# Kernel tuning notes

Hardware: AMD Instinct MI355X
Metric: run time of the kernel (lower is better)

Reference implementation:

```python
import jax, jax.numpy as jnp
import numpy as np

B, H, S, D = 2, 8, 2048, 64  # batch, heads, seq_len, depth (= F_hidden)
LEAKY_SLOPE = 0.2            # tf.nn.leaky_relu default alpha
EPS_ADJ = 1e-9


def setup_inputs() -> dict:
    key = jax.random.key(0)
    ks = jax.random.split(key, 8)
    scale = 1.0 / np.sqrt(D)  # glorot-ish for square [D,D] fan
    return {
        "Hin": jax.random.normal(ks[0], (B, H, S, D), jnp.float32),
        "Hk": jax.random.normal(ks[1], (B, H, S, D), jnp.float32),
        "Hv": jax.random.normal(ks[2], (B, H, S, D), jnp.float32),
        "A": jax.random.normal(ks[3], (B, H, D, D), jnp.float32),
        "mask": jnp.zeros((B, 1, 1, S), jnp.float32),
        "W": jax.random.normal(ks[4], (H, D, D), jnp.float32) * scale,
        "b": jnp.zeros((H, D, D), jnp.float32),
        "a_vec": jax.random.normal(ks[5], (H, D, D), jnp.float32) * scale,
        "ba": jnp.zeros((H, D, D), jnp.float32),
        "pw": jax.random.normal(ks[6], (H, D, D), jnp.float32) * scale,
    }


def reference(Hin, Hk, Hv, A, mask, W, b, a_vec, ba, pw):
    # AW = relu(W @ A + b) + eps          [B,H,D,D]
    AW = jax.nn.relu(jnp.einsum("hfd,bhde->bhfe", W, A) + b[None]) + EPS_ADJ
    # learned power transform on metric tensor
    Ap = AW ** pw[None]                   # [B,H,D,D]
    # energy curvature tensor: a @ Ap + ba
    avAp = jnp.einsum("hfd,bhde->bhfe", a_vec, Ap) + ba[None]  # [B,H,D,D]
    # attention scores: (Hin @ avAp) @ Hk^T / sqrt(dk)
    WHiWHj = jnp.einsum("bhsf,bhfe->bhse", Hin, avAp)          # [B,H,S,D]
    Ep = jnp.einsum("bhse,bhte->bhst", WHiWHj, Hk)             # [B,H,S,S]
    Ep = Ep / jnp.sqrt(jnp.float32(D))
    Ep = jax.nn.leaky_relu(Ep, LEAKY_SLOPE)
    E = jax.nn.softmax(Ep + mask * (-1e9), axis=-1)            # [B,H,S,S]
    # value matmul + output activation (relu); att_head=1 so concat == single head
    H_next = jax.nn.relu(jnp.einsum("bhst,bhtd->bhsd", E, Hv))  # [B,H,S,D]
    return H_next
```

## Files before the change

### kernel.cpp

```cpp
#include <hip/hip_runtime.h>
#include <cmath>

#define B_ 2
#define H_ 8
#define S_ 2048
#define D_ 64
#define TS 64
#define NT (S_ / TS)
#define LDST 68

typedef __attribute__((ext_vector_type(8))) _Float16 f16x8;
typedef __attribute__((ext_vector_type(4))) float f32x4;

__global__ __launch_bounds__(256) void prep_avAp(
    const float* __restrict__ A, const float* __restrict__ W,
    const float* __restrict__ bb, const float* __restrict__ av,
    const float* __restrict__ ba, const float* __restrict__ pw,
    float* __restrict__ avAp)
{
    __shared__ float s0[TS * LDST];
    __shared__ float s1[TS * LDST];
    const int tid = threadIdx.x;
    const int ty = tid >> 4, tx = tid & 15;
    const int bh = blockIdx.x;
    const int h = bh & (H_ - 1);

    const float4* W4 = (const float4*)(W + h * D_ * D_);
    const float4* A4 = (const float4*)(A + bh * D_ * D_);
#pragma unroll
    for (int it = 0; it < 4; ++it) {
        int idx = tid + it * 256;
        int r = idx >> 4, c = idx & 15;
        *(float4*)&s0[r * LDST + c * 4] = W4[idx];
        *(float4*)&s1[r * LDST + c * 4] = A4[idx];
    }
    __syncthreads();

    float acc[4][4] = {};
    for (int d = 0; d < D_; ++d) {
        float4 a4 = *(const float4*)&s1[d * LDST + tx * 4];
#pragma unroll
        for (int i = 0; i < 4; ++i) {
            float w = s0[(ty * 4 + i) * LDST + d];
            acc[i][0] += w * a4.x; acc[i][1] += w * a4.y;
            acc[i][2] += w * a4.z; acc[i][3] += w * a4.w;
        }
    }
    __syncthreads();

#pragma unroll
    for (int i = 0; i < 4; ++i) {
        int f = ty * 4 + i;
        float4 b4 = *(const float4*)&bb[(h * D_ + f) * D_ + tx * 4];
        float4 p4 = *(const float4*)&pw[(h * D_ + f) * D_ + tx * 4];
        float vb[4] = {b4.x, b4.y, b4.z, b4.w};
        float vp[4] = {p4.x, p4.y, p4.z, p4.w};
#pragma unroll
        for (int j = 0; j < 4; ++j) {
            float aw = fmaxf(acc[i][j] + vb[j], 0.f) + 1e-9f;
            s0[f * LDST + tx * 4 + j] = exp2f(vp[j] * __log2f(aw));
        }
    }
    const float4* av4 = (const float4*)(av + h * D_ * D_);
#pragma unroll
    for (int it = 0; it < 4; ++it) {
        int idx = tid + it * 256;
        int r = idx >> 4, c = idx & 15;
        *(float4*)&s1[r * LDST + c * 4] = av4[idx];
    }
    __syncthreads();

    float acc2[4][4] = {};
    for (int d = 0; d < D_; ++d) {
        float4 a4 = *(const float4*)&s0[d * LDST + tx * 4];
#pragma unroll
        for (int i = 0; i < 4; ++i) {
            float w = s1[(ty * 4 + i) * LDST + d];
            acc2[i][0] += w * a4.x; acc2[i][1] += w * a4.y;
            acc2[i][2] += w * a4.z; acc2[i][3] += w * a4.w;
        }
    }
#pragma unroll
    for (int i = 0; i < 4; ++i) {
        int f = ty * 4 + i;
        float4 ba4 = *(const float4*)&ba[(h * D_ + f) * D_ + tx * 4];
        float4 o = make_float4(acc2[i][0] + ba4.x, acc2[i][1] + ba4.y,
                               acc2[i][2] + ba4.z, acc2[i][3] + ba4.w);
        *(float4*)&avAp[bh * D_ * D_ + f * D_ + tx * 4] = o;
    }
}

#define KH_S 0
#define KL_S 8192
#define VT_S 16384
#define P_S  24576
#define MROW_S 32768
#define QP_S 40960
#define AVP_S 0
#define HIN_S 17408
#define SMEM_SZ 58368

__global__ __launch_bounds__(256) void flash4(
    const float* __restrict__ Hin, const float* __restrict__ Hk,
    const float* __restrict__ Hv, const float* __restrict__ maskg,
    const float* __restrict__ avAp, float* __restrict__ out)
{
    __shared__ __align__(16) char smem[SMEM_SZ];
    float* AVP = (float*)(smem + AVP_S);
    float* HIN = (float*)(smem + HIN_S);
    float* QP  = (float*)(smem + QP_S);
    float* MROW = (float*)(smem + MROW_S);

    const int tid = threadIdx.x;
    const int wave = tid >> 6, lane = tid & 63;
    const int l15 = lane & 15, lg = lane >> 4;
    const int qt = blockIdx.x, bh = blockIdx.y;
    const int b = bh >> 3;
    const size_t base = (size_t)bh * S_ * D_;
    const int q0 = qt * TS;

    {
        const float4* a4 = (const float4*)(avAp + bh * D_ * D_);
        const float4* h4 = (const float4*)(Hin + base + (size_t)q0 * D_);
#pragma unroll
        for (int i = 0; i < 4; ++i) {
            int f = tid + i * 256;
            int r = f >> 4, c = (f & 15) * 4;
            *(float4*)&AVP[r * LDST + c] = a4[f];
            *(float4*)&HIN[r * LDST + c] = h4[f];
        }
    }
    __syncthreads();
    {
        const int tx = tid & 15, ty = tid >> 4;
        float acc[4][4] = {};
        for (int d = 0; d < D_; ++d) {
            float4 av = *(const float4*)&AVP[d * LDST + tx * 4];
#pragma unroll
            for (int rr = 0; rr < 4; ++rr) {
                float h = HIN[(ty * 4 + rr) * LDST + d];
                acc[rr][0] += h * av.x; acc[rr][1] += h * av.y;
                acc[rr][2] += h * av.z; acc[rr][3] += h * av.w;
            }
        }
#pragma unroll
        for (int rr = 0; rr < 4; ++rr)
            *(float4*)&QP[(ty * 4 + rr) * LDST + tx * 4] =
                make_float4(acc[rr][0], acc[rr][1], acc[rr][2], acc[rr][3]);
    }
    __syncthreads();

    f16x8 qAh[2], qAl[2];
#pragma unroll
    for (int kc = 0; kc < 2; ++kc) {
        int row = wave * 16 + l15;
        int k0 = kc * 32 + lg * 8;
        float4 v0 = *(const float4*)&QP[row * LDST + k0];
        float4 v1 = *(const float4*)&QP[row * LDST + k0 + 4];
        float xs[8] = {v0.x, v0.y, v0.z, v0.w, v1.x, v1.y, v1.z, v1.w};
#pragma unroll
        for (int j = 0; j < 8; ++j) {
            float x = xs[j] * 0.125f;
            _Float16 hh = (_Float16)x;
            qAh[kc][j] = hh;
            qAl[kc][j] = (_Float16)(x - (float)hh);
        }
    }

    float4 kreg[2][2], vreg[2][2];
    auto stage_load = [&](int kt) {
        const float* Kg = Hk + base + (size_t)kt * TS * D_;
        const float* Vg = Hv + base + (size_t)kt * TS * D_;
#pragma unroll
        for (int i = 0; i < 2; ++i) {
            int c = tid + i * 256;
            kreg[i][0] = *(const float4*)(Kg + c * 8);
            kreg[i][1] = *(const float4*)(Kg + c * 8 + 4);
            vreg[i][0] = *(const float4*)(Vg + c * 8);
            vreg[i][1] = *(const float4*)(Vg + c * 8 + 4);
        }
    };
    auto stage_write = [&]() {
#pragma unroll
        for (int i = 0; i < 2; ++i) {
            int c = tid + i * 256;
            int r = c >> 3, c8 = c & 7;
            float xs[8] = {kreg[i][0].x, kreg[i][0].y, kreg[i][0].z, kreg[i][0].w,
                           kreg[i][1].x, kreg[i][1].y, kreg[i][1].z, kreg[i][1].w};
            f16x8 h, l;
#pragma unroll
            for (int e = 0; e < 8; ++e) {
                _Float16 hh = (_Float16)xs[e];
                h[e] = hh; l[e] = (_Float16)(xs[e] - (float)hh);
            }
            int byte = (r * 128 + c8 * 16) ^ ((r & 7) << 4);
            *(f16x8*)(smem + KH_S + byte) = h;
            *(f16x8*)(smem + KL_S + byte) = l;
            float vs[8] = {vreg[i][0].x, vreg[i][0].y, vreg[i][0].z, vreg[i][0].w,
                           vreg[i][1].x, vreg[i][1].y, vreg[i][1].z, vreg[i][1].w};
#pragma unroll
            for (int e = 0; e < 8; ++e) {
                int vr = c8 * 8 + e;
                int vb = (vr * 128 + r * 2) ^
                         ((((vr & 7) ^ ((vr >> 3) & 7)) << 4));
                *(_Float16*)(smem + VT_S + vb) = (_Float16)vs[e];
            }
        }
    };

    stage_load(0);
    stage_write();
    for (int i = tid; i < S_; i += 256) MROW[i] = -1e9f * maskg[b * S_ + i];
    __syncthreads();

    float mrun[4], lrun[4];
    f32x4 o[4];
#pragma unroll
    for (int i = 0; i < 4; ++i) {
        mrun[i] = -INFINITY; lrun[i] = 0.f;
        o[i] = (f32x4){0.f, 0.f, 0.f, 0.f};
    }

    for (int kt = 0; kt < NT; ++kt) {
        if (kt + 1 < NT) stage_load(kt + 1);

        f32x4 s[4];
#pragma unroll
        for (int ns = 0; ns < 4; ++ns) s[ns] = (f32x4){0.f, 0.f, 0.f, 0.f};
        __builtin_amdgcn_s_setprio(1);
#pragma unroll
        for (int ns = 0; ns < 4; ++ns)
#pragma unroll
            for (int kc = 0; kc < 2; ++kc) {
                int row = ns * 16 + l15;
                int byte = (row * 128 + kc * 64 + lg * 16) ^ ((row & 7) << 4);
                f16x8 kh = *(const f16x8*)(smem + KH_S + byte);
                f16x8 kl = *(const f16x8*)(smem + KL_S + byte);
                s[ns] = __builtin_amdgcn_mfma_f32_16x16x32_f16(qAh[kc], kh, s[ns], 0, 0, 0);
                s[ns] = __builtin_amdgcn_mfma_f32_16x16x32_f16(qAl[kc], kh, s[ns], 0, 0, 0);
                s[ns] = __builtin_amdgcn_mfma_f32_16x16x32_f16(qAh[kc], kl, s[ns], 0, 0, 0);
            }
        __builtin_amdgcn_s_setprio(0);

        float mk[4];
#pragma unroll
        for (int ns = 0; ns < 4; ++ns) mk[ns] = MROW[kt * 64 + ns * 16 + l15];
        float scs[4];
#pragma unroll
        for (int r = 0; r < 4; ++r) {
            float v[4];
#pragma unroll
            for (int ns = 0; ns < 4; ++ns) {
                float x = s[ns][r];
                x = (x > 0.f) ? x : 0.2f * x;
                v[ns] = x + mk[ns];
            }
            float m0 = fmaxf(fmaxf(v[0], v[1]), fmaxf(v[2], v[3]));
#pragma unroll
            for (int off = 1; off < 16; off <<= 1)
                m0 = fmaxf(m0, __shfl_xor(m0, off, 64));
            float mnew = fmaxf(mrun[r], m0);
            float sc = __expf(mrun[r] - mnew);
            mrun[r] = mnew;
            float rs = 0.f;
            float p[4];
#pragma unroll
            for (int ns = 0; ns < 4; ++ns) { p[ns] = __expf(v[ns] - mnew); rs += p[ns]; }
#pragma unroll
            for (int off = 1; off < 16; off <<= 1)
                rs += __shfl_xor(rs, off, 64);
            lrun[r] = lrun[r] * sc + rs;
            scs[r] = sc;
            int prow = lg * 4 + r;
#pragma unroll
            for (int ns = 0; ns < 4; ++ns) {
                int pb = (prow * 128 + (ns * 16 + l15) * 2) ^ ((prow & 7) << 4);
                *(_Float16*)(smem + P_S + wave * 2048 + pb) = (_Float16)p[ns];
            }
        }
#pragma unroll
        for (int ns = 0; ns < 4; ++ns)
#pragma unroll
            for (int r = 0; r < 4; ++r) o[ns][r] *= scs[r];

        __syncthreads();

        __builtin_amdgcn_s_setprio(1);
#pragma unroll
        for (int kc = 0; kc < 2; ++kc) {
            int pb = (l15 * 128 + kc * 64 + lg * 16) ^ ((l15 & 7) << 4);
            f16x8 pf = *(const f16x8*)(smem + P_S + wave * 2048 + pb);
#pragma unroll
            for (int ns = 0; ns < 4; ++ns) {
                int vrow = ns * 16 + l15;
                int vb = (vrow * 128 + kc * 64 + lg * 16) ^
                         ((((vrow & 7) ^ ((vrow >> 3) & 7)) << 4));
                f16x8 vf = *(const f16x8*)(smem + VT_S + vb);
                o[ns] = __builtin_amdgcn_mfma_f32_16x16x32_f16(pf, vf, o[ns], 0, 0, 0);
            }
        }
        __builtin_amdgcn_s_setprio(0);

        __syncthreads();

        if (kt + 1 < NT) stage_write();

        __syncthreads();
    }

#pragma unroll
    for (int r = 0; r < 4; ++r) {
        float inv = 1.f / lrun[r];
        int row = q0 + wave * 16 + lg * 4 + r;
#pragma unroll
        for (int ns = 0; ns < 4; ++ns)
            out[base + (size_t)row * D_ + ns * 16 + l15] =
                fmaxf(o[ns][r] * inv, 0.f);
    }
}

extern "C" void kernel_launch(void* const* d_in, const int* in_sizes, int n_in,
                              void* d_out, int out_size, void* d_ws, size_t ws_size,
                              hipStream_t stream) {
    const float* Hin  = (const float*)d_in[0];
    const float* Hk   = (const float*)d_in[1];
    const float* Hv   = (const float*)d_in[2];
    const float* A    = (const float*)d_in[3];
    const float* mask = (const float*)d_in[4];
    const float* W    = (const float*)d_in[5];
    const float* bb   = (const float*)d_in[6];
    const float* av   = (const float*)d_in[7];
    const float* ba   = (const float*)d_in[8];
    const float* pw   = (const float*)d_in[9];
    float* out = (float*)d_out;
    float* ws  = (float*)d_ws;

    prep_avAp<<<B_ * H_, 256, 0, stream>>>(A, W, bb, av, ba, pw, ws);
    flash4<<<dim3(NT, B_ * H_), 256, 0, stream>>>(Hin, Hk, Hv, mask, ws, out);
}
```

Baseline: 185.9 us.

## Widen KV tile to 128, split K/V prefetch, parallelize prep into two kernels

The flash attention kernel now processes 128 keys per iteration instead of 64, which halves the number of barrier-separated iterations and the online-softmax rescale steps. K and V global loads are issued separately so the V prefetch overlaps the softmax. Shared memory grows to about 72KB, and the larger tiles add register pressure, so occupancy may drop. The prep stage is split into two kernels with a 4x wider grid to spread the small matmuls over more blocks, and the output buffer is used as scratch for the intermediate Ap.

```diff
diff --git a/kernel.cpp b/kernel.cpp
--- a/kernel.cpp
+++ b/kernel.cpp
@@ -6,101 +6,102 @@
 #define S_ 2048
 #define D_ 64
 #define TS 64
-#define NT (S_ / TS)
+#define KV 128
+#define NTT (S_ / KV)
 #define LDST 68
 
 typedef __attribute__((ext_vector_type(8))) _Float16 f16x8;
 typedef __attribute__((ext_vector_type(4))) float f32x4;
 
-__global__ __launch_bounds__(256) void prep_avAp(
+__global__ __launch_bounds__(256) void prep_Ap(
     const float* __restrict__ A, const float* __restrict__ W,
-    const float* __restrict__ bb, const float* __restrict__ av,
-    const float* __restrict__ ba, const float* __restrict__ pw,
-    float* __restrict__ avAp)
+    const float* __restrict__ bb, const float* __restrict__ pw,
+    float* __restrict__ Ap)
 {
-    __shared__ float s0[TS * LDST];
-    __shared__ float s1[TS * LDST];
+    __shared__ float sA[64 * LDST];
+    __shared__ float sW[16 * LDST];
     const int tid = threadIdx.x;
-    const int ty = tid >> 4, tx = tid & 15;
-    const int bh = blockIdx.x;
-    const int h = bh & (H_ - 1);
-
-    const float4* W4 = (const float4*)(W + h * D_ * D_);
-    const float4* A4 = (const float4*)(A + bh * D_ * D_);
+    const int bh = blockIdx.x, h = bh & 7, fs = blockIdx.y << 4;
+
+    const float4* A4 = (const float4*)(A + bh * 4096);
 #pragma unroll
     for (int it = 0; it < 4; ++it) {
         int idx = tid + it * 256;
         int r = idx >> 4, c = idx & 15;
-        *(float4*)&s0[r * LDST + c * 4] = W4[idx];
-        *(float4*)&s1[r * LDST + c * 4] = A4[idx];
-    }
-    __syncthreads();
-
-    float acc[4][4] = {};
-    for (int d = 0; d < D_; ++d) {
-        float4 a4 = *(const float4*)&s1[d * LDST + tx * 4];
-#pragma unroll
-        for (int i = 0; i < 4; ++i) {
-            float w = s0[(ty * 4 + i) * LDST + d];
-            acc[i][0] += w * a4.x; acc[i][1] += w * a4.y;
-            acc[i][2] += w * a4.z; acc[i][3] += w * a4.w;
-        }
-    }
-    __syncthreads();
-
-#pragma unroll
-    for (int i = 0; i < 4; ++i) {
-        int f = ty * 4 + i;
-        float4 b4 = *(const float4*)&bb[(h * D_ + f) * D_ + tx * 4];
-        float4 p4 = *(const float4*)&pw[(h * D_ + f) * D_ + tx * 4];
-        float vb[4] = {b4.x, b4.y, b4.z, b4.w};
-        float vp[4] = {p4.x, p4.y, p4.z, p4.w};
-#pragma unroll
-        for (int j = 0; j < 4; ++j) {
-            float aw = fmaxf(acc[i][j] + vb[j], 0.f) + 1e-9f;
-            s0[f * LDST + tx * 4 + j] = exp2f(vp[j] * __log2f(aw));
-        }
-    }
-    const float4* av4 = (const float4*)(av + h * D_ * D_);
+        *(float4*)&sA[r * LDST + c * 4] = A4[idx];
+    }
+    {
+        int r = tid >> 4, c = tid & 15;
+        *(float4*)&sW[r * LDST + c * 4] =
+            *(const float4*)(W + (h * 64 + fs + r) * 64 + c * 4);
+    }
+    __syncthreads();
+
+    const int ty = tid >> 4, tx = tid & 15;
+    float a0 = 0, a1 = 0, a2 = 0, a3 = 0;
+    for (int d = 0; d < 64; ++d) {
+        float4 a4 = *(const float4*)&sA[d * LDST + tx * 4];
+        float w = sW[ty * LDST + d];
+        a0 += w * a4.x; a1 += w * a4.y; a2 += w * a4.z; a3 += w * a4.w;
+    }
+    int f = fs + ty;
+    float4 b4 = *(const float4*)&bb[(h * 64 + f) * 64 + tx * 4];
+    float4 p4 = *(const float4*)&pw[(h * 64 + f) * 64 + tx * 4];
+    float4 o;
+    o.x = exp2f(p4.x * __log2f(fmaxf(a0 + b4.x, 0.f) + 1e-9f));
+    o.y = exp2f(p4.y * __log2f(fmaxf(a1 + b4.y, 0.f) + 1e-9f));
+    o.z = exp2f(p4.z * __log2f(fmaxf(a2 + b4.z, 0.f) + 1e-9f));
+    o.w = exp2f(p4.w * __log2f(fmaxf(a3 + b4.w, 0.f) + 1e-9f));
+    *(float4*)&Ap[(bh * 64 + f) * 64 + tx * 4] = o;
+}
+
+__global__ __launch_bounds__(256) void prep_avAp2(
+    const float* __restrict__ Ap, const float* __restrict__ av,
+    const float* __restrict__ ba, float* __restrict__ avAp)
+{
+    __shared__ float sA[64 * LDST];
+    __shared__ float sW[16 * LDST];
+    const int tid = threadIdx.x;
+    const int bh = blockIdx.x, h = bh & 7, fs = blockIdx.y << 4;
+
+    const float4* A4 = (const float4*)(Ap + bh * 4096);
 #pragma unroll
     for (int it = 0; it < 4; ++it) {
         int idx = tid + it * 256;
         int r = idx >> 4, c = idx & 15;
-        *(float4*)&s1[r * LDST + c * 4] = av4[idx];
-    }
-    __syncthreads();
-
-    float acc2[4][4] = {};
-    for (int d = 0; d < D_; ++d) {
-        float4 a4 = *(const float4*)&s0[d * LDST + tx * 4];
-#pragma unroll
-        for (int i = 0; i < 4; ++i) {
-            float w = s1[(ty * 4 + i) * LDST + d];
-            acc2[i][0] += w * a4.x; acc2[i][1] += w * a4.y;
-            acc2[i][2] += w * a4.z; acc2[i][3] += w * a4.w;
-        }
-    }
-#pragma unroll
-    for (int i = 0; i < 4; ++i) {
-        int f = ty * 4 + i;
-        float4 ba4 = *(const float4*)&ba[(h * D_ + f) * D_ + tx * 4];
-        float4 o = make_float4(acc2[i][0] + ba4.x, acc2[i][1] + ba4.y,
-                               acc2[i][2] + ba4.z, acc2[i][3] + ba4.w);
-        *(float4*)&avAp[bh * D_ * D_ + f * D_ + tx * 4] = o;
-    }
+        *(float4*)&sA[r * LDST + c * 4] = A4[idx];
+    }
+    {
+        int r = tid >> 4, c = tid & 15;
+        *(float4*)&sW[r * LDST + c * 4] =
+            *(const float4*)(av + (h * 64 + fs + r) * 64 + c * 4);
+    }
+    __syncthreads();
+
+    const int ty = tid >> 4, tx = tid & 15;
+    float a0 = 0, a1 = 0, a2 = 0, a3 = 0;
+    for (int d = 0; d < 64; ++d) {
+        float4 a4 = *(const float4*)&sA[d * LDST + tx * 4];
+        float w = sW[ty * LDST + d];
+        a0 += w * a4.x; a1 += w * a4.y; a2 += w * a4.z; a3 += w * a4.w;
+    }
+    int f = fs + ty;
+    float4 b4 = *(const float4*)&ba[(h * 64 + f) * 64 + tx * 4];
+    *(float4*)&avAp[(bh * 64 + f) * 64 + tx * 4] =
+        make_float4(a0 + b4.x, a1 + b4.y, a2 + b4.z, a3 + b4.w);
 }
 
 #define KH_S 0
-#define KL_S 8192
-#define VT_S 16384
-#define P_S  24576
-#define MROW_S 32768
-#define QP_S 40960
+#define KL_S 16384
+#define VT_S 32768
+#define P_S  49152
+#define MROW_S 65536
+#define QP_S 34816
 #define AVP_S 0
 #define HIN_S 17408
-#define SMEM_SZ 58368
-
-__global__ __launch_bounds__(256) void flash4(
+#define SMEM_SZ 73728
+
+__global__ __launch_bounds__(256) void flash5(
     const float* __restrict__ Hin, const float* __restrict__ Hk,
     const float* __restrict__ Hv, const float* __restrict__ maskg,
     const float* __restrict__ avAp, float* __restrict__ out)
@@ -166,23 +167,30 @@
             qAl[kc][j] = (_Float16)(x - (float)hh);
         }
     }
-
-    float4 kreg[2][2], vreg[2][2];
-    auto stage_load = [&](int kt) {
-        const float* Kg = Hk + base + (size_t)kt * TS * D_;
-        const float* Vg = Hv + base + (size_t)kt * TS * D_;
-#pragma unroll
-        for (int i = 0; i < 2; ++i) {
+    __syncthreads();
+
+    float4 kreg[4][2], vreg[4][2];
+    auto stage_load_K = [&](int kt) {
+        const float* Kg = Hk + base + (size_t)kt * KV * D_;
+#pragma unroll
+        for (int i = 0; i < 4; ++i) {
             int c = tid + i * 256;
             kreg[i][0] = *(const float4*)(Kg + c * 8);
             kreg[i][1] = *(const float4*)(Kg + c * 8 + 4);
+        }
+    };
+    auto stage_load_V = [&](int kt) {
+        const float* Vg = Hv + base + (size_t)kt * KV * D_;
+#pragma unroll
+        for (int i = 0; i < 4; ++i) {
+            int c = tid + i * 256;
             vreg[i][0] = *(const float4*)(Vg + c * 8);
             vreg[i][1] = *(const float4*)(Vg + c * 8 + 4);
         }
     };
     auto stage_write = [&]() {
 #pragma unroll
-        for (int i = 0; i < 2; ++i) {
+        for (int i = 0; i < 4; ++i) {
             int c = tid + i * 256;
             int r = c >> 3, c8 = c & 7;
             float xs[8] = {kreg[i][0].x, kreg[i][0].y, kreg[i][0].z, kreg[i][0].w,
@@ -201,14 +209,15 @@
 #pragma unroll
             for (int e = 0; e < 8; ++e) {
                 int vr = c8 * 8 + e;
-                int vb = (vr * 128 + r * 2) ^
+                int vb = (vr * 256 + r * 2) ^
                          ((((vr & 7) ^ ((vr >> 3) & 7)) << 4));
                 *(_Float16*)(smem + VT_S + vb) = (_Float16)vs[e];
             }
         }
     };
 
-    stage_load(0);
+    stage_load_K(0);
+    stage_load_V(0);
     stage_write();
     for (int i = tid; i < S_; i += 256) MROW[i] = -1e9f * maskg[b * S_ + i];
     __syncthreads();
@@ -221,15 +230,15 @@
         o[i] = (f32x4){0.f, 0.f, 0.f, 0.f};
     }
 
-    for (int kt = 0; kt < NT; ++kt) {
-        if (kt + 1 < NT) stage_load(kt + 1);
-
-        f32x4 s[4];
-#pragma unroll
-        for (int ns = 0; ns < 4; ++ns) s[ns] = (f32x4){0.f, 0.f, 0.f, 0.f};
+    for (int kt = 0; kt < NTT; ++kt) {
+        if (kt + 1 < NTT) stage_load_K(kt + 1);
+
+        f32x4 s[8];
+#pragma unroll
+        for (int ns = 0; ns < 8; ++ns) s[ns] = (f32x4){0.f, 0.f, 0.f, 0.f};
         __builtin_amdgcn_s_setprio(1);
 #pragma unroll
-        for (int ns = 0; ns < 4; ++ns)
+        for (int ns = 0; ns < 8; ++ns)
 #pragma unroll
             for (int kc = 0; kc < 2; ++kc) {
                 int row = ns * 16 + l15;
@@ -242,20 +251,23 @@
             }
         __builtin_amdgcn_s_setprio(0);
 
-        float mk[4];
-#pragma unroll
-        for (int ns = 0; ns < 4; ++ns) mk[ns] = MROW[kt * 64 + ns * 16 + l15];
+        if (kt + 1 < NTT) stage_load_V(kt + 1);
+
+        float mk[8];
+#pragma unroll
+        for (int ns = 0; ns < 8; ++ns) mk[ns] = MROW[kt * KV + ns * 16 + l15];
         float scs[4];
 #pragma unroll
         for (int r = 0; r < 4; ++r) {
-            float v[4];
-#pragma unroll
-            for (int ns = 0; ns < 4; ++ns) {
+            float v[8];
+#pragma unroll
+            for (int ns = 0; ns < 8; ++ns) {
                 float x = s[ns][r];
                 x = (x > 0.f) ? x : 0.2f * x;
                 v[ns] = x + mk[ns];
             }
-            float m0 = fmaxf(fmaxf(v[0], v[1]), fmaxf(v[2], v[3]));
+            float m0 = fmaxf(fmaxf(fmaxf(v[0], v[1]), fmaxf(v[2], v[3])),
+                             fmaxf(fmaxf(v[4], v[5]), fmaxf(v[6], v[7])));
 #pragma unroll
             for (int off = 1; off < 16; off <<= 1)
                 m0 = fmaxf(m0, __shfl_xor(m0, off, 64));
@@ -263,9 +275,9 @@
             float sc = __expf(mrun[r] - mnew);
             mrun[r] = mnew;
             float rs = 0.f;
-            float p[4];
-#pragma unroll
-            for (int ns = 0; ns < 4; ++ns) { p[ns] = __expf(v[ns] - mnew); rs += p[ns]; }
+            float p[8];
+#pragma unroll
+            for (int ns = 0; ns < 8; ++ns) { p[ns] = __expf(v[ns] - mnew); rs += p[ns]; }
 #pragma unroll
             for (int off = 1; off < 16; off <<= 1)
                 rs += __shfl_xor(rs, off, 64);
@@ -273,9 +285,9 @@
             scs[r] = sc;
             int prow = lg * 4 + r;
 #pragma unroll
-            for (int ns = 0; ns < 4; ++ns) {
-                int pb = (prow * 128 + (ns * 16 + l15) * 2) ^ ((prow & 7) << 4);
-                *(_Float16*)(smem + P_S + wave * 2048 + pb) = (_Float16)p[ns];
+            for (int ns = 0; ns < 8; ++ns) {
+                int pb = (prow * 256 + (ns * 16 + l15) * 2) ^ ((prow & 7) << 4);
+                *(_Float16*)(smem + P_S + wave * 4096 + pb) = (_Float16)p[ns];
             }
         }
 #pragma unroll
@@ -287,13 +299,13 @@
 
         __builtin_amdgcn_s_setprio(1);
 #pragma unroll
-        for (int kc = 0; kc < 2; ++kc) {
-            int pb = (l15 * 128 + kc * 64 + lg * 16) ^ ((l15 & 7) << 4);
-            f16x8 pf = *(const f16x8*)(smem + P_S + wave * 2048 + pb);
+        for (int kc = 0; kc < 4; ++kc) {
+            int pb = (l15 * 256 + kc * 64 + lg * 16) ^ ((l15 & 7) << 4);
+            f16x8 pf = *(const f16x8*)(smem + P_S + wave * 4096 + pb);
 #pragma unroll
             for (int ns = 0; ns < 4; ++ns) {
                 int vrow = ns * 16 + l15;
-                int vb = (vrow * 128 + kc * 64 + lg * 16) ^
+                int vb = (vrow * 256 + kc * 64 + lg * 16) ^
                          ((((vrow & 7) ^ ((vrow >> 3) & 7)) << 4));
                 f16x8 vf = *(const f16x8*)(smem + VT_S + vb);
                 o[ns] = __builtin_amdgcn_mfma_f32_16x16x32_f16(pf, vf, o[ns], 0, 0, 0);
@@ -303,7 +315,7 @@
 
         __syncthreads();
 
-        if (kt + 1 < NT) stage_write();
+        if (kt + 1 < NTT) stage_write();
 
         __syncthreads();
     }
@@ -334,7 +346,9 @@
     const float* pw   = (const float*)d_in[9];
     float* out = (float*)d_out;
     float* ws  = (float*)d_ws;
-
-    prep_avAp<<<B_ * H_, 256, 0, stream>>>(A, W, bb, av, ba, pw, ws);
-    flash4<<<dim3(NT, B_ * H_), 256, 0, stream>>>(Hin, Hk, Hv, mask, ws, out);
+    float* ApS = out;
+
+    prep_Ap<<<dim3(B_ * H_, 4), 256, 0, stream>>>(A, W, bb, pw, ApS);
+    prep_avAp2<<<dim3(B_ * H_, 4), 256, 0, stream>>>(ApS, av, ba, ws);
+    flash5<<<dim3(S_ / TS, B_ * H_), 256, 0, stream>>>(Hin, Hk, Hv, mask, ws, out);
 }
```

Result: slower. 228.5 us (+22.9%).
